# Optimization experiments

Hardware: AMD Instinct MI355X
Metric: run time of the kernel (lower is better)

The kernel has to match this reference:

```python
import jax, jax.numpy as jnp
import numpy as np
from jax import lax

B, L, D_MODEL = 2, 1024, 1024
EXPAND, D_STATE, D_CONV = 2, 16, 4
D_INNER = EXPAND * D_MODEL
DT_RANK = D_MODEL // 16  # ceil(1024/16) = 64
D_FF = 4 * D_MODEL


def setup_inputs() -> dict:
    key = jax.random.key(0)
    ks = jax.random.split(key, 20)
    s = lambda *sh: 1.0 / np.sqrt(sh[-1])
    inp = {
        "x": jax.random.normal(ks[0], (B, L, D_MODEL), jnp.float32),
        "ln1_w": jnp.ones((D_MODEL,), jnp.float32),
        "ln1_b": jnp.zeros((D_MODEL,), jnp.float32),
        "W_in": jax.random.normal(ks[1], (2 * D_INNER, D_MODEL), jnp.float32) * s(D_MODEL),
        "conv_w": jax.random.normal(ks[2], (D_INNER, D_CONV), jnp.float32) * s(D_CONV),
        "conv_b": jnp.zeros((D_INNER,), jnp.float32),
        "W_xproj": jax.random.normal(ks[3], (DT_RANK + 2 * D_STATE, D_INNER), jnp.float32) * s(D_INNER),
        "W_dt": jax.random.normal(ks[4], (D_INNER, DT_RANK), jnp.float32) * s(DT_RANK),
        "b_dt": jax.random.uniform(ks[5], (D_INNER,), jnp.float32, -4.0, -2.0),  # dt bias ~ small softplus
        "A_log": jnp.log(jnp.broadcast_to(jnp.arange(1, D_STATE + 1, dtype=jnp.float32), (D_INNER, D_STATE))),
        "D": jnp.ones((D_INNER,), jnp.float32),
        "W_out": jax.random.normal(ks[6], (D_MODEL, D_INNER), jnp.float32) * s(D_INNER),
        "ln2_w": jnp.ones((D_MODEL,), jnp.float32),
        "ln2_b": jnp.zeros((D_MODEL,), jnp.float32),
        "W1": jax.random.normal(ks[7], (D_FF, D_MODEL), jnp.float32) * s(D_MODEL),
        "b1": jnp.zeros((D_FF,), jnp.float32),
        "W2": jax.random.normal(ks[8], (D_MODEL, D_FF), jnp.float32) * s(D_FF),
        "b2": jnp.zeros((D_MODEL,), jnp.float32),
    }
    return inp


def _layernorm(x, w, b, eps=1e-5):
    mu = jnp.mean(x, axis=-1, keepdims=True)
    var = jnp.var(x, axis=-1, keepdims=True)
    return (x - mu) * lax.rsqrt(var + eps) * w + b


def _mamba(h, W_in, conv_w, conv_b, W_xproj, W_dt, b_dt, A_log, D, W_out):
    # in_proj -> [B, L, 2*d_inner]
    xz = jnp.einsum("bld,ed->ble", h, W_in)
    u, z = xz[..., :D_INNER], xz[..., D_INNER:]
    # causal depthwise conv over time
    uc = jnp.transpose(u, (0, 2, 1))  # [B, d_inner, L]
    uc = lax.conv_general_dilated(
        uc, conv_w[:, None, :], window_strides=(1,), padding=[(D_CONV - 1, 0)],
        dimension_numbers=("NCH", "OIH", "NCH"), feature_group_count=D_INNER)
    uc = jax.nn.silu(uc + conv_b[None, :, None])
    u = jnp.transpose(uc, (0, 2, 1))  # [B, L, d_inner]
    # input-dependent dt, B, C
    x_db = jnp.einsum("bld,ed->ble", u, W_xproj)
    dt = jax.nn.softplus(jnp.einsum("blr,dr->bld", x_db[..., :DT_RANK], W_dt) + b_dt)
    Bm = x_db[..., DT_RANK:DT_RANK + D_STATE]  # [B, L, d_state]
    Cm = x_db[..., DT_RANK + D_STATE:]         # [B, L, d_state]
    A = -jnp.exp(A_log)                        # [d_inner, d_state]

    def step(hst, t):
        dt_t, B_t, C_t, u_t = t  # [B,d_inner], [B,ds], [B,ds], [B,d_inner]
        dA = jnp.exp(dt_t[:, :, None] * A)                       # [B,d_inner,d_state]
        hst = dA * hst + dt_t[:, :, None] * B_t[:, None, :] * u_t[:, :, None]
        y_t = jnp.einsum("bds,bs->bd", hst, C_t)
        return hst, y_t

    h0 = jnp.zeros((u.shape[0], D_INNER, D_STATE), u.dtype)
    xs = (jnp.swapaxes(dt, 0, 1), jnp.swapaxes(Bm, 0, 1), jnp.swapaxes(Cm, 0, 1), jnp.swapaxes(u, 0, 1))
    _, ys = lax.scan(step, h0, xs)
    y = jnp.swapaxes(ys, 0, 1) + u * D  # skip term D*u
    y = y * jax.nn.silu(z)
    return jnp.einsum("ble,de->bld", y, W_out)


def reference(x, ln1_w, ln1_b, W_in, conv_w, conv_b, W_xproj, W_dt, b_dt, A_log, D,
              W_out, ln2_w, ln2_b, W1, b1, W2, b2):
    x = x + _mamba(_layernorm(x, ln1_w, ln1_b), W_in, conv_w, conv_b, W_xproj, W_dt, b_dt, A_log, D, W_out)
    h = _layernorm(x, ln2_w, ln2_b)
    ffn = jnp.einsum("blf,df->bld", jax.nn.relu(jnp.einsum("bld,fd->blf", h, W1) + b1), W2) + b2
    return x + ffn
```

## Files before the change

### kernel.cpp

```cpp
#include <hip/hip_runtime.h>

typedef unsigned short u16;
typedef unsigned int   u32;
typedef short   bf16x8 __attribute__((ext_vector_type(8)));
typedef float   f32x4  __attribute__((ext_vector_type(4)));
typedef u16     u16x4  __attribute__((ext_vector_type(4)));

__device__ __forceinline__ u16 f2b(float f) {
    u32 u = __builtin_bit_cast(u32, f);
    u32 r = u + 0x7FFFu + ((u >> 16) & 1u);
    return (u16)(r >> 16);
}
__device__ __forceinline__ float b2f(u16 h) {
    u32 u = ((u32)h) << 16;
    return __builtin_bit_cast(float, u);
}
__device__ __forceinline__ u16x4 f4_to_b4(float4 v) {
    u16x4 o; o.x = f2b(v.x); o.y = f2b(v.y); o.z = f2b(v.z); o.w = f2b(v.w);
    return o;
}

__device__ __forceinline__ float fexp2(float x) {
    float r;
    asm("v_exp_f32 %0, %1" : "=v"(r) : "v"(x));
    return r;
}
__device__ __forceinline__ float flog2(float x) {
    float r;
    asm("v_log_f32 %0, %1" : "=v"(r) : "v"(x));
    return r;
}

template <int CTRL>
__device__ __forceinline__ float dpp_add(float p) {
    int pi = __builtin_bit_cast(int, p);
    int q  = __builtin_amdgcn_update_dpp(pi, pi, CTRL, 0xF, 0xF, false);
    return p + __builtin_bit_cast(float, q);
}
#define DPP_XOR1 0xB1
#define DPP_XOR2 0x4E
#define DPP_HMIR 0x141
#define DPP_MIR  0x140

#define MROWS   2048
#define NSEG    16
#define SEGT    64
#define L2E     1.44269504088896340736f
#define LN2     0.69314718055994530942f

#define GLDS(g, l) __builtin_amdgcn_global_load_lds(                      \
    (const __attribute__((address_space(1))) void*)(g),                   \
    (__attribute__((address_space(3))) void*)(l), 16, 0, 0)

__global__ __launch_bounds__(256) void cvt_kernel(const float* __restrict__ in,
                                                  u16* __restrict__ out, int n4) {
    int i = blockIdx.x * 256 + threadIdx.x;
    if (i < n4) {
        float4 v = ((const float4*)in)[i];
        ((u16x4*)out)[i] = f4_to_b4(v);
    }
}

__global__ __launch_bounds__(256) void pad_xproj_kernel(const float* __restrict__ in,
                                                        u16* __restrict__ out) {
    int i = blockIdx.x * 256 + threadIdx.x;
    int r = i >> 9, c4 = i & 511;
    float4 v = make_float4(0.f, 0.f, 0.f, 0.f);
    if (r < 96) v = ((const float4*)(in + (size_t)r * 2048))[c4];
    ((u16x4*)(out + (size_t)r * 2048))[c4] = f4_to_b4(v);
}

__global__ __launch_bounds__(256) void ln_kernel(const float* __restrict__ x,
                                                 const float* __restrict__ w,
                                                 const float* __restrict__ b,
                                                 u16* __restrict__ out) {
    const int row = blockIdx.x;
    const int tid = threadIdx.x;
    const float4 v = ((const float4*)(x + (size_t)row * 1024))[tid];
    float s = v.x + v.y + v.z + v.w;
    float q = v.x * v.x + v.y * v.y + v.z * v.z + v.w * v.w;
#pragma unroll
    for (int off = 1; off < 64; off <<= 1) {
        s += __shfl_xor(s, off, 64);
        q += __shfl_xor(q, off, 64);
    }
    __shared__ float ss[4], qq[4];
    const int wave = tid >> 6;
    if ((tid & 63) == 0) { ss[wave] = s; qq[wave] = q; }
    __syncthreads();
    s = ss[0] + ss[1] + ss[2] + ss[3];
    q = qq[0] + qq[1] + qq[2] + qq[3];
    const float mean = s * (1.f / 1024.f);
    const float var  = q * (1.f / 1024.f) - mean * mean;
    const float rstd = rsqrtf(var + 1e-5f);
    const float4 wv = ((const float4*)w)[tid];
    const float4 bv = ((const float4*)b)[tid];
    float4 o;
    o.x = (v.x - mean) * rstd * wv.x + bv.x;
    o.y = (v.y - mean) * rstd * wv.y + bv.y;
    o.z = (v.z - mean) * rstd * wv.z + bv.z;
    o.w = (v.w - mean) * rstd * wv.w + bv.w;
    ((u16x4*)(out + (size_t)row * 1024))[tid] = f4_to_b4(o);
}

__global__ __launch_bounds__(256) void conv_kernel(const float* __restrict__ xzu,
                                                   const float* __restrict__ cw,
                                                   const float* __restrict__ cb,
                                                   u16* __restrict__ up,
                                                   u16* __restrict__ utl) {
    const int idx = blockIdx.x * 256 + threadIdx.x;
    const int row = idx >> 9;
    const int d4  = idx & 511;
    const int d   = d4 * 4;
    const int bb  = row >> 10;
    const int t   = row & 1023;
    float w0[4], w1[4], w2[4], w3[4];
    *(float4*)w0 = ((const float4*)cw)[d + 0];
    *(float4*)w1 = ((const float4*)cw)[d + 1];
    *(float4*)w2 = ((const float4*)cw)[d + 2];
    *(float4*)w3 = ((const float4*)cw)[d + 3];
    float4 a = ((const float4*)cb)[d4];
#pragma unroll
    for (int j = 0; j < 4; ++j) {
        const int tt = t - 3 + j;
        if (tt >= 0) {
            const float4 uv = *(const float4*)(xzu + ((size_t)(bb * 1024 + tt)) * 2048 + d);
            a.x += uv.x * w0[j];
            a.y += uv.y * w1[j];
            a.z += uv.z * w2[j];
            a.w += uv.w * w3[j];
        }
    }
    float4 o;
    o.x = a.x / (1.f + __expf(-a.x));
    o.y = a.y / (1.f + __expf(-a.y));
    o.z = a.z / (1.f + __expf(-a.z));
    o.w = a.w / (1.f + __expf(-a.w));
    const u16x4 pk = f4_to_b4(o);
    ((u16x4*)up)[idx] = pk;
    *(u16x4*)(utl + (((size_t)(d >> 4)) * 2048 + row) * 16 + (d & 15)) = pk;
}

template <int EPI>
__global__ __launch_bounds__(256) void gemm_tb(const u16* __restrict__ A,
                                               const u16* __restrict__ Bw,
                                               void* __restrict__ Cptr,
                                               void* __restrict__ Cptr2,
                                               const float* __restrict__ bias,
                                               int M, int N, int K, int KS) {
    const int nbm = gridDim.x, nbn = gridDim.y;
    const int nwg = nbm * nbn;
    const int id  = blockIdx.x + nbm * blockIdx.y;
    const int sw  = (id & 7) * (nwg >> 3) + (id >> 3);
    const int bm  = sw % nbm, bn = sw / nbm;

    __shared__ u16 Asm[3][128 * 32];
    __shared__ u16 Bsm[3][128 * 32];
    const int tid  = threadIdx.x;
    const int kz   = blockIdx.z;
    const int lane = tid & 63;
    const int wave = tid >> 6;
    const int wm   = wave >> 1, wn = wave & 1;
    const u16* Ag = A  + (size_t)bm * 128 * K;
    const u16* Bg = Bw + (size_t)bn * 128 * K;
    const int r0 = tid >> 2;
    const int r1 = r0 + 64;
    const int sg = (tid & 3) * 8;
    const int k0 = kz * KS;
    const int nk = KS >> 5;
    const int fr = lane & 15, fk = (lane >> 4) * 8;

#define STG(bf, kk)                                                            \
    {                                                                          \
        const int kof = k0 + (kk) * 32;                                        \
        GLDS(Ag + (size_t)r0 * K + kof + sg, &Asm[bf][tid * 8]);               \
        GLDS(Ag + (size_t)r1 * K + kof + sg, &Asm[bf][(tid + 256) * 8]);       \
        GLDS(Bg + (size_t)r0 * K + kof + sg, &Bsm[bf][tid * 8]);               \
        GLDS(Bg + (size_t)r1 * K + kof + sg, &Bsm[bf][(tid + 256) * 8]);       \
    }

    f32x4 acc[4][4] = {};
    STG(0, 0); STG(1, 1); STG(2, 2);
    int buf = 0;
    for (int k = 0; k < nk; ++k) {
        if (k < nk - 2)       asm volatile("s_waitcnt vmcnt(8)" ::: "memory");
        else if (k == nk - 2) asm volatile("s_waitcnt vmcnt(4)" ::: "memory");
        else                  asm volatile("s_waitcnt vmcnt(0)" ::: "memory");
        __builtin_amdgcn_s_barrier();
        bf16x8 a[4], b[4];
#pragma unroll
        for (int m = 0; m < 4; ++m)
            a[m] = *(const bf16x8*)&Asm[buf][(wm * 64 + m * 16 + fr) * 32 + fk];
#pragma unroll
        for (int n = 0; n < 4; ++n)
            b[n] = *(const bf16x8*)&Bsm[buf][(wn * 64 + n * 16 + fr) * 32 + fk];
        asm volatile("s_waitcnt lgkmcnt(0)" ::: "memory");
        __builtin_amdgcn_s_barrier();
        if (k + 3 < nk) STG(buf, k + 3);
#pragma unroll
        for (int m = 0; m < 4; ++m)
#pragma unroll
            for (int n = 0; n < 4; ++n)
                acc[m][n] = __builtin_amdgcn_mfma_f32_16x16x32_bf16(a[m], b[n], acc[m][n], 0, 0, 0);
        buf = (buf == 2) ? 0 : buf + 1;
    }
#undef STG

    const int fq = lane >> 4;
#pragma unroll
    for (int m = 0; m < 4; ++m) {
#pragma unroll
        for (int n = 0; n < 4; ++n) {
            const int row0 = bm * 128 + wm * 64 + m * 16 + fq * 4;
            const int col  = bn * 128 + wn * 64 + n * 16 + fr;
#pragma unroll
            for (int j = 0; j < 4; ++j) {
                float v = acc[m][n][j];
                if constexpr (EPI == 3) {
                    v += bias[col];
                    ((u16*)Cptr)[(size_t)(row0 + j) * N + col] = f2b(fmaxf(v, 0.f));
                } else if constexpr (EPI == 5) {
                    if (col < 2048) {
                        ((float*)Cptr)[(size_t)(row0 + j) * 2048 + col] = v;
                    } else {
                        const float sv = v / (1.f + __expf(-v));
                        const int zc = col - 2048;
                        ((u16*)Cptr2)[(((size_t)(zc >> 4)) * 2048 + row0 + j) * 16 + (zc & 15)]
                            = f2b(sv);
                    }
                } else {
                    ((float*)Cptr)[(size_t)kz * M * N + (size_t)(row0 + j) * N + col] = v;
                }
            }
        }
    }
}

__global__ __launch_bounds__(256) void xproj_combine(const float* __restrict__ part,
                                                     u16* __restrict__ xdbr,
                                                     float* __restrict__ bcp) {
    int i = blockIdx.x * 256 + threadIdx.x;
    int row = i >> 5, c4 = i & 31;
    if (c4 >= 24) return;
    float4 s = make_float4(0.f, 0.f, 0.f, 0.f);
#pragma unroll
    for (int p = 0; p < 8; ++p) {
        float4 v = ((const float4*)(part + (size_t)p * MROWS * 128 + (size_t)row * 128))[c4];
        s.x += v.x; s.y += v.y; s.z += v.z; s.w += v.w;
    }
    if (c4 < 16) {
        ((u16x4*)(xdbr + (size_t)row * 64))[c4] = f4_to_b4(s);
    } else {
        const int e0 = (c4 - 16) * 4;
        float sv[4] = {s.x, s.y, s.z, s.w};
#pragma unroll
        for (int j = 0; j < 4; ++j) {
            const int e = e0 + j;
            const int st  = (e < 16) ? e : (e - 16);
            const int isc = (e < 16) ? 0 : 1;
            bcp[(size_t)(row >> 1) * 64 + st * 4 + (row & 1) * 2 + isc] = sv[j];
        }
    }
}

__device__ __forceinline__ void compute_dtu_tile(const u16* __restrict__ xdbr,
                                                 const u16* __restrict__ Wdtb,
                                                 const float* __restrict__ b_dt,
                                                 const u16* __restrict__ utile,
                                                 float* __restrict__ du_s,
                                                 size_t t0, int d0, int w, int l) {
    const int fr = l & 15, fk = (l >> 4) * 8;
    const bf16x8 a0 = *(const bf16x8*)(xdbr + (t0 + w * 16 + fr) * 64 + fk);
    const bf16x8 a1 = *(const bf16x8*)(xdbr + (t0 + w * 16 + fr) * 64 + 32 + fk);
    const bf16x8 b0 = *(const bf16x8*)(Wdtb + (size_t)(d0 + fr) * 64 + fk);
    const bf16x8 b1 = *(const bf16x8*)(Wdtb + (size_t)(d0 + fr) * 64 + 32 + fk);
    const float bdt = b_dt[d0 + fr];
    f32x4 acc = {};
    acc = __builtin_amdgcn_mfma_f32_16x16x32_bf16(a0, b0, acc, 0, 0, 0);
    acc = __builtin_amdgcn_mfma_f32_16x16x32_bf16(a1, b1, acc, 0, 0, 0);
#pragma unroll
    for (int j = 0; j < 4; ++j) {
        const int row = w * 16 + (l >> 4) * 4 + j;
        float v = acc[j] + bdt;
        const float sp = flog2(1.f + fexp2(v * L2E)) * LN2;
        v = (v > 20.f) ? v : sp;
        const float uval = b2f(utile[(t0 + row) * 16 + fr]);
        float2 dv; dv.x = v; dv.y = v * uval;
        *(float2*)&du_s[(row >> 1) * 66 + fr * 4 + (row & 1) * 2] = dv;
    }
}

__device__ __forceinline__ void stage_bc(const float* __restrict__ bcp,
                                         float* __restrict__ bc_s,
                                         size_t p0, int w, int l) {
    const int pr = (w << 3) + (l >> 4);
    const int pc = (l & 15) << 2;
    GLDS(bcp + (p0 + pr) * 64 + pc,     &bc_s[(w << 9)]);
    GLDS(bcp + (p0 + pr + 4) * 64 + pc, &bc_s[(w << 9) + 256]);
}

__global__ __launch_bounds__(256) void scan_pass1(const u16* __restrict__ xdbr,
                                                  const u16* __restrict__ Wdtb,
                                                  const float* __restrict__ b_dt,
                                                  const u16* __restrict__ utl,
                                                  const float* __restrict__ bcp,
                                                  const float* __restrict__ A_log,
                                                  float* __restrict__ Qarr,
                                                  float* __restrict__ Sarr) {
    __shared__ __align__(16) float du_s[32 * 66];
    __shared__ __align__(16) float bc_s[32 * 64];

    const int tid = threadIdx.x;
    const int l   = tid & 63;
    const int w   = tid >> 6;
    const int s   = l & 15;
    const int g   = (w << 2) | (l >> 4);
    const int d0  = blockIdx.x << 4;
    const int b   = blockIdx.y;
    const int seg = blockIdx.z;
    const int d   = d0 + g;
    const size_t t0 = (size_t)b * 1024 + (size_t)seg * SEGT;
    const u16* utile = utl + (size_t)(d0 >> 4) * 2048 * 16;

    stage_bc(bcp, bc_s, t0 >> 1, w, l);
    compute_dtu_tile(xdbr, Wdtb, b_dt, utile, du_s, t0, d0, w, l);

    const float As2 = -__expf(A_log[d * 16 + s]) * L2E;
    asm volatile("s_waitcnt vmcnt(0) lgkmcnt(0)" ::: "memory");
    __builtin_amdgcn_s_barrier();

    float Q = 0.f, S = 0.f;
#pragma unroll 8
    for (int t2 = 0; t2 < 32; ++t2) {
        const float4 du4 = *(const float4*)&du_s[t2 * 66 + g * 4];
        const float4 BC2 = *(const float4*)&bc_s[t2 * 64 + s * 4];
        S += du4.x;
        Q = fexp2(du4.x * As2) * Q + du4.y * BC2.x;
        S += du4.z;
        Q = fexp2(du4.z * As2) * Q + du4.w * BC2.z;
    }
    Qarr[(((size_t)seg * 2 + b) * 2048 + d) * 16 + s] = Q;
    if (s == 0) Sarr[((size_t)seg * 2 + b) * 2048 + d] = S;
}

__global__ __launch_bounds__(256) void scan_prefix(const float* __restrict__ Qarr,
                                                   const float* __restrict__ Sarr,
                                                   const float* __restrict__ A_log,
                                                   float* __restrict__ H0) {
    const int tid = threadIdx.x;
    const int d   = (blockIdx.x << 4) + (tid >> 4);
    const int s   = tid & 15;
    const int b   = blockIdx.y;
    const float As2 = -__expf(A_log[d * 16 + s]) * L2E;
    float h = 0.f;
#pragma unroll
    for (int i = 0; i < NSEG; ++i) {
        const size_t base = ((size_t)i * 2 + b) * 2048 + d;
        H0[base * 16 + s] = h;
        h = fexp2(As2 * Sarr[base]) * h + Qarr[base * 16 + s];
    }
}

__global__ __launch_bounds__(256) void scan_pass2(const u16* __restrict__ xdbr,
                                                  const u16* __restrict__ Wdtb,
                                                  const float* __restrict__ b_dt,
                                                  const u16* __restrict__ utl,
                                                  const float* __restrict__ bcp,
                                                  const u16* __restrict__ zst,
                                                  const float* __restrict__ A_log,
                                                  const float* __restrict__ Dp,
                                                  const float* __restrict__ H0,
                                                  u16* __restrict__ ymul) {
    __shared__ __align__(16) float du_s[32 * 66];
    __shared__ __align__(16) float bc_s[32 * 64];
    __shared__ __align__(16) u16   u_s[1024];
    __shared__ __align__(16) u16   z_s[1024];

    const int tid = threadIdx.x;
    const int l   = tid & 63;
    const int w   = tid >> 6;
    const int s   = l & 15;
    const int g   = (w << 2) | (l >> 4);
    const int d0  = blockIdx.x << 4;
    const int b   = blockIdx.y;
    const int seg = blockIdx.z;
    const int d   = d0 + g;
    const size_t t0 = (size_t)b * 1024 + (size_t)seg * SEGT;
    const u16* utile = utl + (size_t)(d0 >> 4) * 2048 * 16;
    const u16* ztile = zst + (size_t)(d0 >> 4) * 2048 * 16;

    stage_bc(bcp, bc_s, t0 >> 1, w, l);
    if (w < 2)
        GLDS(utile + t0 * 16 + ((w & 1) * 64 + l) * 8, &u_s[(w & 1) << 9]);
    else
        GLDS(ztile + t0 * 16 + ((w & 1) * 64 + l) * 8, &z_s[(w & 1) << 9]);

    compute_dtu_tile(xdbr, Wdtb, b_dt, utile, du_s, t0, d0, w, l);

    const float As2 = -__expf(A_log[d * 16 + s]) * L2E;
    float h = H0[(((size_t)seg * 2 + b) * 2048 + d) * 16 + s];

    asm volatile("s_waitcnt vmcnt(0) lgkmcnt(0)" ::: "memory");
    __builtin_amdgcn_s_barrier();

    float pk[4];
#pragma unroll
    for (int c = 0; c < 4; ++c) {
        pk[c] = 0.f;
#pragma unroll
        for (int q = 0; q < 8; ++q) {
            const int t2 = c * 8 + q;
            const float4 du4 = *(const float4*)&du_s[t2 * 66 + g * 4];
            const float4 BC2 = *(const float4*)&bc_s[t2 * 64 + s * 4];
            h = fexp2(du4.x * As2) * h + du4.y * BC2.x;
            float p = h * BC2.y;
            p = dpp_add<DPP_XOR1>(p);
            p = dpp_add<DPP_XOR2>(p);
            p = dpp_add<DPP_HMIR>(p);
            p = dpp_add<DPP_MIR>(p);
            {
                const unsigned long long km = 0x0001000100010001ULL << (2 * q);
                asm("v_cndmask_b32 %0, %0, %1, %2" : "+v"(pk[c]) : "v"(p), "s"(km));
            }
            h = fexp2(du4.z * As2) * h + du4.w * BC2.z;
            p = h * BC2.w;
            p = dpp_add<DPP_XOR1>(p);
            p = dpp_add<DPP_XOR2>(p);
            p = dpp_add<DPP_HMIR>(p);
            p = dpp_add<DPP_MIR>(p);
            {
                const unsigned long long km = 0x0001000100010001ULL << (2 * q + 1);
                asm("v_cndmask_b32 %0, %0, %1, %2" : "+v"(pk[c]) : "v"(p), "s"(km));
            }
        }
    }

    __builtin_amdgcn_s_barrier();
    float* p_s = du_s;
#pragma unroll
    for (int c = 0; c < 4; ++c) {
        const int row = c * 16 + s;
        p_s[row * 16 + (g ^ (row & 12))] = pk[c];
    }

    asm volatile("s_waitcnt lgkmcnt(0)" ::: "memory");
    __builtin_amdgcn_s_barrier();

    {
        const int tt = tid >> 2, cc = (tid & 3) << 2;
        const float4 pv = *(const float4*)&p_s[tt * 16 + (cc ^ (tt & 12))];
        const u16x4  uv = *(const u16x4*)&u_s[tt * 16 + cc];
        const u16x4  zs = *(const u16x4*)&z_s[tt * 16 + cc];
        const float4 Dv = *(const float4*)(Dp + d0 + cc);
        float4 o;
        o.x = (pv.x + b2f(uv.x) * Dv.x) * b2f(zs.x);
        o.y = (pv.y + b2f(uv.y) * Dv.y) * b2f(zs.y);
        o.z = (pv.z + b2f(uv.z) * Dv.z) * b2f(zs.z);
        o.w = (pv.w + b2f(uv.w) * Dv.w) * b2f(zs.w);
        *(u16x4*)(ymul + (t0 + tt) * 2048 + d0 + cc) = f4_to_b4(o);
    }
}

__global__ __launch_bounds__(256) void ffn2_combine(const float* __restrict__ part,
                                                    const float* __restrict__ x2,
                                                    const float* __restrict__ b2,
                                                    float* __restrict__ out) {
    int i = blockIdx.x * 256 + threadIdx.x;
    float4 s = ((const float4*)x2)[i];
    float4 bv = ((const float4*)b2)[i & 255];
    s.x += bv.x; s.y += bv.y; s.z += bv.z; s.w += bv.w;
#pragma unroll
    for (int p = 0; p < 4; ++p) {
        float4 v = ((const float4*)(part + (size_t)p * MROWS * 1024))[i];
        s.x += v.x; s.y += v.y; s.z += v.z; s.w += v.w;
    }
    ((float4*)out)[i] = s;
}

__global__ __launch_bounds__(256) void outproj_combine_ln2(const float* __restrict__ x,
                                                           const float* __restrict__ part,
                                                           const float* __restrict__ w,
                                                           const float* __restrict__ b,
                                                           float* __restrict__ x2,
                                                           u16* __restrict__ h2) {
    const int row = blockIdx.x;
    const int tid = threadIdx.x;
    float4 v = ((const float4*)(x + (size_t)row * 1024))[tid];
    float4 p0 = ((const float4*)(part + (size_t)row * 1024))[tid];
    float4 p1 = ((const float4*)(part + (size_t)MROWS * 1024 + (size_t)row * 1024))[tid];
    v.x += p0.x + p1.x; v.y += p0.y + p1.y; v.z += p0.z + p1.z; v.w += p0.w + p1.w;
    ((float4*)(x2 + (size_t)row * 1024))[tid] = v;
    float s = v.x + v.y + v.z + v.w;
    float q = v.x * v.x + v.y * v.y + v.z * v.z + v.w * v.w;
#pragma unroll
    for (int off = 1; off < 64; off <<= 1) {
        s += __shfl_xor(s, off, 64);
        q += __shfl_xor(q, off, 64);
    }
    __shared__ float ss[4], qq[4];
    const int wave = tid >> 6;
    if ((tid & 63) == 0) { ss[wave] = s; qq[wave] = q; }
    __syncthreads();
    s = ss[0] + ss[1] + ss[2] + ss[3];
    q = qq[0] + qq[1] + qq[2] + qq[3];
    const float mean = s * (1.f / 1024.f);
    const float var  = q * (1.f / 1024.f) - mean * mean;
    const float rstd = rsqrtf(var + 1e-5f);
    const float4 wv = ((const float4*)w)[tid];
    const float4 bv = ((const float4*)b)[tid];
    float4 o;
    o.x = (v.x - mean) * rstd * wv.x + bv.x;
    o.y = (v.y - mean) * rstd * wv.y + bv.y;
    o.z = (v.z - mean) * rstd * wv.z + bv.z;
    o.w = (v.w - mean) * rstd * wv.w + bv.w;
    ((u16x4*)(h2 + (size_t)row * 1024))[tid] = f4_to_b4(o);
}

extern "C" void kernel_launch(void* const* d_in, const int* in_sizes, int n_in,
                              void* d_out, int out_size, void* d_ws, size_t ws_size,
                              hipStream_t stream) {
    const float* x      = (const float*)d_in[0];
    const float* ln1_w  = (const float*)d_in[1];
    const float* ln1_b  = (const float*)d_in[2];
    const float* W_in   = (const float*)d_in[3];
    const float* conv_w = (const float*)d_in[4];
    const float* conv_b = (const float*)d_in[5];
    const float* W_xproj= (const float*)d_in[6];
    const float* W_dt   = (const float*)d_in[7];
    const float* b_dt   = (const float*)d_in[8];
    const float* A_log  = (const float*)d_in[9];
    const float* Dvec   = (const float*)d_in[10];
    const float* W_out  = (const float*)d_in[11];
    const float* ln2_w  = (const float*)d_in[12];
    const float* ln2_b  = (const float*)d_in[13];
    const float* W1     = (const float*)d_in[14];
    const float* b1     = (const float*)d_in[15];
    const float* W2     = (const float*)d_in[16];
    const float* b2     = (const float*)d_in[17];
    float* out = (float*)d_out;
    char*  ws  = (char*)d_ws;
    const size_t MB = 1024ull * 1024ull;

    u16*   h1b   = (u16*)(ws + 0);
    float* xzu   = (float*)(ws + 4 * MB);
    u16*   zst   = (u16*)(ws + 20 * MB);
    u16*   upb   = (u16*)(ws + 28 * MB);
    u16*   utl   = (u16*)(ws + 36 * MB);
    float* parts = (float*)(ws + 44 * MB);
    float* bcp   = (float*)(ws + 52 * MB);
    u16*   xdbr  = (u16*)(ws + 52 * MB + 256 * 1024);
    u16*   Wdtb  = (u16*)(ws + 52 * MB + 512 * 1024);
    u16*   ymul  = (u16*)(ws + 53 * MB);
    float* Qarr  = (float*)(ws + 61 * MB);
    float* Sarr  = (float*)(ws + 65 * MB);
    float* H0    = (float*)(ws + 66 * MB);
    float* x2    = (float*)(ws + 70 * MB);
    u16*   Winb  = (u16*)(ws + 78 * MB);
    u16*   Woutb = (u16*)(ws + 86 * MB);
    u16*   W1b   = (u16*)(ws + 90 * MB);
    u16*   W2b   = (u16*)(ws + 98 * MB);
    u16*   Wxpb  = (u16*)(ws + 106 * MB);
    u16*   h2b   = h1b;
    float* opart = (float*)(ws + 4 * MB);
    u16*   f1    = (u16*)(ws + 4 * MB);
    float* fpart = (float*)(ws + 20 * MB);

    cvt_kernel<<<4096, 256, 0, stream>>>(W_in,  Winb,  4096 * 1024 / 4);
    cvt_kernel<<<2048, 256, 0, stream>>>(W_out, Woutb, 1024 * 2048 / 4);
    cvt_kernel<<<4096, 256, 0, stream>>>(W1,    W1b,   4096 * 1024 / 4);
    cvt_kernel<<<4096, 256, 0, stream>>>(W2,    W2b,   1024 * 4096 / 4);
    cvt_kernel<<<128,  256, 0, stream>>>(W_dt,  Wdtb,  2048 * 64 / 4);
    pad_xproj_kernel<<<256, 256, 0, stream>>>(W_xproj, Wxpb);

    ln_kernel<<<2048, 256, 0, stream>>>(x, ln1_w, ln1_b, h1b);
    gemm_tb<5><<<dim3(16, 32, 1), 256, 0, stream>>>(h1b, Winb, xzu, zst, nullptr,
                                                    MROWS, 4096, 1024, 1024);
    conv_kernel<<<4096, 256, 0, stream>>>(xzu, conv_w, conv_b, upb, utl);
    gemm_tb<10><<<dim3(16, 1, 8), 256, 0, stream>>>(upb, Wxpb, parts, nullptr, nullptr,
                                                    MROWS, 128, 2048, 256);
    xproj_combine<<<256, 256, 0, stream>>>(parts, xdbr, bcp);
    scan_pass1<<<dim3(128, 2, NSEG), 256, 0, stream>>>(xdbr, Wdtb, b_dt, utl, bcp, A_log,
                                                       Qarr, Sarr);
    scan_prefix<<<dim3(128, 2), 256, 0, stream>>>(Qarr, Sarr, A_log, H0);
    scan_pass2<<<dim3(128, 2, NSEG), 256, 0, stream>>>(xdbr, Wdtb, b_dt, utl, bcp, zst,
                                                       A_log, Dvec, H0, ymul);
    gemm_tb<10><<<dim3(16, 8, 2), 256, 0, stream>>>(ymul, Woutb, opart, nullptr, nullptr,
                                                    MROWS, 1024, 2048, 1024);
    outproj_combine_ln2<<<2048, 256, 0, stream>>>(x, opart, ln2_w, ln2_b, x2, h2b);
    gemm_tb<3><<<dim3(16, 32, 1), 256, 0, stream>>>(h2b, W1b, f1, nullptr, b1,
                                                    MROWS, 4096, 1024, 1024);
    gemm_tb<10><<<dim3(16, 8, 4), 256, 0, stream>>>(f1, W2b, fpart, nullptr, nullptr,
                                                    MROWS, 1024, 4096, 1024);
    ffn2_combine<<<2048, 256, 0, stream>>>(fpart, x2, b2, out);
}
```

Measured before the change: 234.7 us.

## Replace split-K GEMMs with 64x64-tile GEMM fusing residual and bias epilogue

Adds a 64x64-tile bf16 MFMA GEMM with a three-stage LDS pipeline that writes output plus residual (and bias) directly. It replaces the split-K out_proj and FFN2 GEMMs and their combine kernels, so the fp32 partial buffers are never written and re-read and two launches are dropped. LN2 now runs through the generic ln_kernel on x2. The cost is more tiles, each with a full-length K loop (2048 or 4096), and less data reuse per tile than the 128-wide version.

```diff
diff --git a/kernel.cpp b/kernel.cpp
--- a/kernel.cpp
+++ b/kernel.cpp
@@ -230,6 +230,95 @@
                     }
                 } else {
                     ((float*)Cptr)[(size_t)kz * M * N + (size_t)(row0 + j) * N + col] = v;
+                }
+            }
+        }
+    }
+}
+
+template <int EPI>
+__global__ __launch_bounds__(256) void gemm64(const u16* __restrict__ A,
+                                              const u16* __restrict__ Bw,
+                                              float* __restrict__ Cptr,
+                                              const float* __restrict__ bias,
+                                              const float* __restrict__ resid,
+                                              int M, int N, int K) {
+    const int nbm = gridDim.x, nbn = gridDim.y;
+    const int nwg = nbm * nbn;
+    const int id  = blockIdx.x + nbm * blockIdx.y;
+    const int sw  = (id & 7) * (nwg >> 3) + (id >> 3);
+    const int bm  = sw % nbm, bn = sw / nbm;
+
+    __shared__ u16 Asm[3][2][64 * 32];
+    __shared__ u16 Bsm[3][2][64 * 32];
+    const int tid  = threadIdx.x;
+    const int lane = tid & 63;
+    const int wave = tid >> 6;
+    const int wm   = wave >> 1, wn = wave & 1;
+    const u16* Ag = A  + (size_t)bm * 64 * K;
+    const u16* Bg = Bw + (size_t)bn * 64 * K;
+    const int r0 = tid >> 2;
+    const int sg = (tid & 3) * 8;
+    const int nk = K >> 6;
+    const int fr = lane & 15, fk = (lane >> 4) * 8;
+
+#define STG64(bf, kk)                                                          \
+    {                                                                          \
+        const int kof = (kk) * 64;                                             \
+        GLDS(Ag + (size_t)r0 * K + kof + sg,      &Asm[bf][0][tid * 8]);       \
+        GLDS(Ag + (size_t)r0 * K + kof + 32 + sg, &Asm[bf][1][tid * 8]);       \
+        GLDS(Bg + (size_t)r0 * K + kof + sg,      &Bsm[bf][0][tid * 8]);       \
+        GLDS(Bg + (size_t)r0 * K + kof + 32 + sg, &Bsm[bf][1][tid * 8]);       \
+    }
+
+    f32x4 acc[2][2] = {};
+    STG64(0, 0); STG64(1, 1); STG64(2, 2);
+    int buf = 0;
+    for (int k = 0; k < nk; ++k) {
+        if (k < nk - 2)       asm volatile("s_waitcnt vmcnt(8)" ::: "memory");
+        else if (k == nk - 2) asm volatile("s_waitcnt vmcnt(4)" ::: "memory");
+        else                  asm volatile("s_waitcnt vmcnt(0)" ::: "memory");
+        __builtin_amdgcn_s_barrier();
+        bf16x8 a[2][2], b[2][2];
+#pragma unroll
+        for (int kk = 0; kk < 2; ++kk) {
+#pragma unroll
+            for (int m = 0; m < 2; ++m)
+                a[kk][m] = *(const bf16x8*)&Asm[buf][kk][(wm * 32 + m * 16 + fr) * 32 + fk];
+#pragma unroll
+            for (int n = 0; n < 2; ++n)
+                b[kk][n] = *(const bf16x8*)&Bsm[buf][kk][(wn * 32 + n * 16 + fr) * 32 + fk];
+        }
+        asm volatile("s_waitcnt lgkmcnt(0)" ::: "memory");
+        __builtin_amdgcn_s_barrier();
+        if (k + 3 < nk) STG64(buf, k + 3);
+#pragma unroll
+        for (int kk = 0; kk < 2; ++kk)
+#pragma unroll
+            for (int m = 0; m < 2; ++m)
+#pragma unroll
+                for (int n = 0; n < 2; ++n)
+                    acc[m][n] = __builtin_amdgcn_mfma_f32_16x16x32_bf16(a[kk][m], b[kk][n],
+                                                                        acc[m][n], 0, 0, 0);
+        buf = (buf == 2) ? 0 : buf + 1;
+    }
+#undef STG64
+
+    const int fq = lane >> 4;
+#pragma unroll
+    for (int m = 0; m < 2; ++m) {
+#pragma unroll
+        for (int n = 0; n < 2; ++n) {
+            const int row0 = bm * 64 + wm * 32 + m * 16 + fq * 4;
+            const int col  = bn * 64 + wn * 32 + n * 16 + fr;
+#pragma unroll
+            for (int j = 0; j < 4; ++j) {
+                float v = acc[m][n][j];
+                const size_t off = (size_t)(row0 + j) * N + col;
+                if constexpr (EPI == 6) {
+                    Cptr[off] = v + bias[col] + resid[off];
+                } else {
+                    Cptr[off] = v + resid[off];
                 }
             }
         }
@@ -461,61 +550,6 @@
     }
 }
 
-__global__ __launch_bounds__(256) void ffn2_combine(const float* __restrict__ part,
-                                                    const float* __restrict__ x2,
-                                                    const float* __restrict__ b2,
-                                                    float* __restrict__ out) {
-    int i = blockIdx.x * 256 + threadIdx.x;
-    float4 s = ((const float4*)x2)[i];
-    float4 bv = ((const float4*)b2)[i & 255];
-    s.x += bv.x; s.y += bv.y; s.z += bv.z; s.w += bv.w;
-#pragma unroll
-    for (int p = 0; p < 4; ++p) {
-        float4 v = ((const float4*)(part + (size_t)p * MROWS * 1024))[i];
-        s.x += v.x; s.y += v.y; s.z += v.z; s.w += v.w;
-    }
-    ((float4*)out)[i] = s;
-}
-
-__global__ __launch_bounds__(256) void outproj_combine_ln2(const float* __restrict__ x,
-                                                           const float* __restrict__ part,
-                                                           const float* __restrict__ w,
-                                                           const float* __restrict__ b,
-                                                           float* __restrict__ x2,
-                                                           u16* __restrict__ h2) {
-    const int row = blockIdx.x;
-    const int tid = threadIdx.x;
-    float4 v = ((const float4*)(x + (size_t)row * 1024))[tid];
-    float4 p0 = ((const float4*)(part + (size_t)row * 1024))[tid];
-    float4 p1 = ((const float4*)(part + (size_t)MROWS * 1024 + (size_t)row * 1024))[tid];
-    v.x += p0.x + p1.x; v.y += p0.y + p1.y; v.z += p0.z + p1.z; v.w += p0.w + p1.w;
-    ((float4*)(x2 + (size_t)row * 1024))[tid] = v;
-    float s = v.x + v.y + v.z + v.w;
-    float q = v.x * v.x + v.y * v.y + v.z * v.z + v.w * v.w;
-#pragma unroll
-    for (int off = 1; off < 64; off <<= 1) {
-        s += __shfl_xor(s, off, 64);
-        q += __shfl_xor(q, off, 64);
-    }
-    __shared__ float ss[4], qq[4];
-    const int wave = tid >> 6;
-    if ((tid & 63) == 0) { ss[wave] = s; qq[wave] = q; }
-    __syncthreads();
-    s = ss[0] + ss[1] + ss[2] + ss[3];
-    q = qq[0] + qq[1] + qq[2] + qq[3];
-    const float mean = s * (1.f / 1024.f);
-    const float var  = q * (1.f / 1024.f) - mean * mean;
-    const float rstd = rsqrtf(var + 1e-5f);
-    const float4 wv = ((const float4*)w)[tid];
-    const float4 bv = ((const float4*)b)[tid];
-    float4 o;
-    o.x = (v.x - mean) * rstd * wv.x + bv.x;
-    o.y = (v.y - mean) * rstd * wv.y + bv.y;
-    o.z = (v.z - mean) * rstd * wv.z + bv.z;
-    o.w = (v.w - mean) * rstd * wv.w + bv.w;
-    ((u16x4*)(h2 + (size_t)row * 1024))[tid] = f4_to_b4(o);
-}
-
 extern "C" void kernel_launch(void* const* d_in, const int* in_sizes, int n_in,
                               void* d_out, int out_size, void* d_ws, size_t ws_size,
                               hipStream_t stream) {
@@ -561,9 +595,7 @@
     u16*   W2b   = (u16*)(ws + 98 * MB);
     u16*   Wxpb  = (u16*)(ws + 106 * MB);
     u16*   h2b   = h1b;
-    float* opart = (float*)(ws + 4 * MB);
     u16*   f1    = (u16*)(ws + 4 * MB);
-    float* fpart = (float*)(ws + 20 * MB);
 
     cvt_kernel<<<4096, 256, 0, stream>>>(W_in,  Winb,  4096 * 1024 / 4);
     cvt_kernel<<<2048, 256, 0, stream>>>(W_out, Woutb, 1024 * 2048 / 4);
@@ -584,12 +616,11 @@
     scan_prefix<<<dim3(128, 2), 256, 0, stream>>>(Qarr, Sarr, A_log, H0);
     scan_pass2<<<dim3(128, 2, NSEG), 256, 0, stream>>>(xdbr, Wdtb, b_dt, utl, bcp, zst,
                                                        A_log, Dvec, H0, ymul);
-    gemm_tb<10><<<dim3(16, 8, 2), 256, 0, stream>>>(ymul, Woutb, opart, nullptr, nullptr,
-                                                    MROWS, 1024, 2048, 1024);
-    outproj_combine_ln2<<<2048, 256, 0, stream>>>(x, opart, ln2_w, ln2_b, x2, h2b);
+    gemm64<7><<<dim3(32, 16), 256, 0, stream>>>(ymul, Woutb, x2, nullptr, x,
+                                                MROWS, 1024, 2048);
+    ln_kernel<<<2048, 256, 0, stream>>>(x2, ln2_w, ln2_b, h2b);
     gemm_tb<3><<<dim3(16, 32, 1), 256, 0, stream>>>(h2b, W1b, f1, nullptr, b1,
                                                     MROWS, 4096, 1024, 1024);
-    gemm_tb<10><<<dim3(16, 8, 4), 256, 0, stream>>>(f1, W2b, fpart, nullptr, nullptr,
-                                                    MROWS, 1024, 4096, 1024);
-    ffn2_combine<<<2048, 256, 0, stream>>>(fpart, x2, b2, out);
-}
+    gemm64<6><<<dim3(32, 16), 256, 0, stream>>>(f1, W2b, out, b2, x2,
+                                                MROWS, 1024, 4096);
+}
```

Result: no change. 238.7 us (+1.7%).

## Use 64x128 tiles for the wide GEMMs and store the in_proj u-half as bf16

Applied to the files above, without the earlier changes.

Adds a gemm_a64 kernel with a 64-row by 128-column tile, launched as a 32x32 grid, for the in_proj and FFN1 GEMMs (N=4096). This gives 1024 workgroups instead of 512, which should fill the CUs better. The u half of the in_proj output is now written as bf16 instead of fp32, and the conv kernel reads bf16, halving that intermediate's memory traffic. The split-K gemm_tb is reduced to plain fp32 partial output. The cost is lower data reuse per tile and an extra bf16 rounding of u before the convolution.

```diff
diff --git a/kernel.cpp b/kernel.cpp
--- a/kernel.cpp
+++ b/kernel.cpp
@@ -103,7 +103,7 @@
     ((u16x4*)(out + (size_t)row * 1024))[tid] = f4_to_b4(o);
 }
 
-__global__ __launch_bounds__(256) void conv_kernel(const float* __restrict__ xzu,
+__global__ __launch_bounds__(256) void conv_kernel(const u16* __restrict__ xzu,
                                                    const float* __restrict__ cw,
                                                    const float* __restrict__ cb,
                                                    u16* __restrict__ up,
@@ -124,11 +124,11 @@
     for (int j = 0; j < 4; ++j) {
         const int tt = t - 3 + j;
         if (tt >= 0) {
-            const float4 uv = *(const float4*)(xzu + ((size_t)(bb * 1024 + tt)) * 2048 + d);
-            a.x += uv.x * w0[j];
-            a.y += uv.y * w1[j];
-            a.z += uv.z * w2[j];
-            a.w += uv.w * w3[j];
+            const u16x4 uv = *(const u16x4*)(xzu + ((size_t)(bb * 1024 + tt)) * 2048 + d);
+            a.x += b2f(uv.x) * w0[j];
+            a.y += b2f(uv.y) * w1[j];
+            a.z += b2f(uv.z) * w2[j];
+            a.w += b2f(uv.w) * w3[j];
         }
     }
     float4 o;
@@ -141,17 +141,14 @@
     *(u16x4*)(utl + (((size_t)(d >> 4)) * 2048 + row) * 16 + (d & 15)) = pk;
 }
 
-template <int EPI>
 __global__ __launch_bounds__(256) void gemm_tb(const u16* __restrict__ A,
                                                const u16* __restrict__ Bw,
-                                               void* __restrict__ Cptr,
-                                               void* __restrict__ Cptr2,
-                                               const float* __restrict__ bias,
+                                               float* __restrict__ Cptr,
                                                int M, int N, int K, int KS) {
     const int nbm = gridDim.x, nbn = gridDim.y;
     const int nwg = nbm * nbn;
     const int id  = blockIdx.x + nbm * blockIdx.y;
-    const int sw  = (id & 7) * (nwg >> 3) + (id >> 3);
+    const int sw  = (nwg >= 8) ? ((id & 7) * (nwg >> 3) + (id >> 3)) : id;
     const int bm  = sw % nbm, bn = sw / nbm;
 
     __shared__ u16 Asm[3][128 * 32];
@@ -214,22 +211,96 @@
             const int row0 = bm * 128 + wm * 64 + m * 16 + fq * 4;
             const int col  = bn * 128 + wn * 64 + n * 16 + fr;
 #pragma unroll
+            for (int j = 0; j < 4; ++j)
+                Cptr[(size_t)kz * M * N + (size_t)(row0 + j) * N + col] = acc[m][n][j];
+        }
+    }
+}
+
+template <int EPI>
+__global__ __launch_bounds__(256) void gemm_a64(const u16* __restrict__ A,
+                                                const u16* __restrict__ Bw,
+                                                void* __restrict__ Cptr,
+                                                void* __restrict__ Cptr2,
+                                                const float* __restrict__ bias,
+                                                int M, int N, int K) {
+    const int nbm = gridDim.x, nbn = gridDim.y;
+    const int nwg = nbm * nbn;
+    const int id  = blockIdx.x + nbm * blockIdx.y;
+    const int sw  = (id & 7) * (nwg >> 3) + (id >> 3);
+    const int bm  = sw % nbm, bn = sw / nbm;
+
+    __shared__ u16 Asm[3][64 * 32];
+    __shared__ u16 Bsm[3][128 * 32];
+    const int tid  = threadIdx.x;
+    const int lane = tid & 63;
+    const int wave = tid >> 6;
+    const int wm   = wave >> 1, wn = wave & 1;
+    const u16* Ag = A  + (size_t)bm * 64 * K;
+    const u16* Bg = Bw + (size_t)bn * 128 * K;
+    const int r0 = tid >> 2;
+    const int r1 = r0 + 64;
+    const int sg = (tid & 3) * 8;
+    const int nk = K >> 5;
+    const int fr = lane & 15, fk = (lane >> 4) * 8;
+
+#define STGA(bf, kk)                                                           \
+    {                                                                          \
+        const int kof = (kk) * 32;                                             \
+        GLDS(Ag + (size_t)r0 * K + kof + sg, &Asm[bf][tid * 8]);               \
+        GLDS(Bg + (size_t)r0 * K + kof + sg, &Bsm[bf][tid * 8]);               \
+        GLDS(Bg + (size_t)r1 * K + kof + sg, &Bsm[bf][(tid + 256) * 8]);       \
+    }
+
+    f32x4 acc[2][4] = {};
+    STGA(0, 0); STGA(1, 1); STGA(2, 2);
+    int buf = 0;
+    for (int k = 0; k < nk; ++k) {
+        if (k < nk - 2)       asm volatile("s_waitcnt vmcnt(6)" ::: "memory");
+        else if (k == nk - 2) asm volatile("s_waitcnt vmcnt(3)" ::: "memory");
+        else                  asm volatile("s_waitcnt vmcnt(0)" ::: "memory");
+        __builtin_amdgcn_s_barrier();
+        bf16x8 a[2], b[4];
+#pragma unroll
+        for (int m = 0; m < 2; ++m)
+            a[m] = *(const bf16x8*)&Asm[buf][(wm * 32 + m * 16 + fr) * 32 + fk];
+#pragma unroll
+        for (int n = 0; n < 4; ++n)
+            b[n] = *(const bf16x8*)&Bsm[buf][(wn * 64 + n * 16 + fr) * 32 + fk];
+        asm volatile("s_waitcnt lgkmcnt(0)" ::: "memory");
+        __builtin_amdgcn_s_barrier();
+        if (k + 3 < nk) STGA(buf, k + 3);
+#pragma unroll
+        for (int m = 0; m < 2; ++m)
+#pragma unroll
+            for (int n = 0; n < 4; ++n)
+                acc[m][n] = __builtin_amdgcn_mfma_f32_16x16x32_bf16(a[m], b[n], acc[m][n], 0, 0, 0);
+        buf = (buf == 2) ? 0 : buf + 1;
+    }
+#undef STGA
+
+    const int fq = lane >> 4;
+#pragma unroll
+    for (int m = 0; m < 2; ++m) {
+#pragma unroll
+        for (int n = 0; n < 4; ++n) {
+            const int row0 = bm * 64 + wm * 32 + m * 16 + fq * 4;
+            const int col  = bn * 128 + wn * 64 + n * 16 + fr;
+#pragma unroll
             for (int j = 0; j < 4; ++j) {
                 float v = acc[m][n][j];
                 if constexpr (EPI == 3) {
                     v += bias[col];
                     ((u16*)Cptr)[(size_t)(row0 + j) * N + col] = f2b(fmaxf(v, 0.f));
-                } else if constexpr (EPI == 5) {
+                } else {
                     if (col < 2048) {
-                        ((float*)Cptr)[(size_t)(row0 + j) * 2048 + col] = v;
+                        ((u16*)Cptr)[(size_t)(row0 + j) * 2048 + col] = f2b(v);
                     } else {
                         const float sv = v / (1.f + __expf(-v));
                         const int zc = col - 2048;
                         ((u16*)Cptr2)[(((size_t)(zc >> 4)) * 2048 + row0 + j) * 16 + (zc & 15)]
                             = f2b(sv);
                     }
-                } else {
-                    ((float*)Cptr)[(size_t)kz * M * N + (size_t)(row0 + j) * N + col] = v;
                 }
             }
         }
@@ -542,24 +613,24 @@
     const size_t MB = 1024ull * 1024ull;
 
     u16*   h1b   = (u16*)(ws + 0);
-    float* xzu   = (float*)(ws + 4 * MB);
-    u16*   zst   = (u16*)(ws + 20 * MB);
-    u16*   upb   = (u16*)(ws + 28 * MB);
-    u16*   utl   = (u16*)(ws + 36 * MB);
-    float* parts = (float*)(ws + 44 * MB);
-    float* bcp   = (float*)(ws + 52 * MB);
-    u16*   xdbr  = (u16*)(ws + 52 * MB + 256 * 1024);
-    u16*   Wdtb  = (u16*)(ws + 52 * MB + 512 * 1024);
-    u16*   ymul  = (u16*)(ws + 53 * MB);
-    float* Qarr  = (float*)(ws + 61 * MB);
-    float* Sarr  = (float*)(ws + 65 * MB);
-    float* H0    = (float*)(ws + 66 * MB);
-    float* x2    = (float*)(ws + 70 * MB);
-    u16*   Winb  = (u16*)(ws + 78 * MB);
-    u16*   Woutb = (u16*)(ws + 86 * MB);
-    u16*   W1b   = (u16*)(ws + 90 * MB);
-    u16*   W2b   = (u16*)(ws + 98 * MB);
-    u16*   Wxpb  = (u16*)(ws + 106 * MB);
+    u16*   xzu   = (u16*)(ws + 4 * MB);
+    u16*   zst   = (u16*)(ws + 12 * MB);
+    u16*   upb   = (u16*)(ws + 20 * MB);
+    u16*   utl   = (u16*)(ws + 28 * MB);
+    float* parts = (float*)(ws + 36 * MB);
+    float* bcp   = (float*)(ws + 44 * MB);
+    u16*   xdbr  = (u16*)(ws + 44 * MB + 256 * 1024);
+    u16*   Wdtb  = (u16*)(ws + 44 * MB + 512 * 1024);
+    u16*   ymul  = (u16*)(ws + 45 * MB);
+    float* Qarr  = (float*)(ws + 53 * MB);
+    float* Sarr  = (float*)(ws + 57 * MB);
+    float* H0    = (float*)(ws + 58 * MB);
+    float* x2    = (float*)(ws + 62 * MB);
+    u16*   Winb  = (u16*)(ws + 70 * MB);
+    u16*   Woutb = (u16*)(ws + 78 * MB);
+    u16*   W1b   = (u16*)(ws + 82 * MB);
+    u16*   W2b   = (u16*)(ws + 90 * MB);
+    u16*   Wxpb  = (u16*)(ws + 98 * MB);
     u16*   h2b   = h1b;
     float* opart = (float*)(ws + 4 * MB);
     u16*   f1    = (u16*)(ws + 4 * MB);
@@ -573,23 +644,20 @@
     pad_xproj_kernel<<<256, 256, 0, stream>>>(W_xproj, Wxpb);
 
     ln_kernel<<<2048, 256, 0, stream>>>(x, ln1_w, ln1_b, h1b);
-    gemm_tb<5><<<dim3(16, 32, 1), 256, 0, stream>>>(h1b, Winb, xzu, zst, nullptr,
-                                                    MROWS, 4096, 1024, 1024);
+    gemm_a64<5><<<dim3(32, 32), 256, 0, stream>>>(h1b, Winb, xzu, zst, nullptr,
+                                                  MROWS, 4096, 1024);
     conv_kernel<<<4096, 256, 0, stream>>>(xzu, conv_w, conv_b, upb, utl);
-    gemm_tb<10><<<dim3(16, 1, 8), 256, 0, stream>>>(upb, Wxpb, parts, nullptr, nullptr,
-                                                    MROWS, 128, 2048, 256);
+    gemm_tb<<<dim3(16, 1, 8), 256, 0, stream>>>(upb, Wxpb, parts, MROWS, 128, 2048, 256);
     xproj_combine<<<256, 256, 0, stream>>>(parts, xdbr, bcp);
     scan_pass1<<<dim3(128, 2, NSEG), 256, 0, stream>>>(xdbr, Wdtb, b_dt, utl, bcp, A_log,
                                                        Qarr, Sarr);
     scan_prefix<<<dim3(128, 2), 256, 0, stream>>>(Qarr, Sarr, A_log, H0);
     scan_pass2<<<dim3(128, 2, NSEG), 256, 0, stream>>>(xdbr, Wdtb, b_dt, utl, bcp, zst,
                                                        A_log, Dvec, H0, ymul);
-    gemm_tb<10><<<dim3(16, 8, 2), 256, 0, stream>>>(ymul, Woutb, opart, nullptr, nullptr,
-                                                    MROWS, 1024, 2048, 1024);
+    gemm_tb<<<dim3(16, 8, 2), 256, 0, stream>>>(ymul, Woutb, opart, MROWS, 1024, 2048, 1024);
     outproj_combine_ln2<<<2048, 256, 0, stream>>>(x, opart, ln2_w, ln2_b, x2, h2b);
-    gemm_tb<3><<<dim3(16, 32, 1), 256, 0, stream>>>(h2b, W1b, f1, nullptr, b1,
-                                                    MROWS, 4096, 1024, 1024);
-    gemm_tb<10><<<dim3(16, 8, 4), 256, 0, stream>>>(f1, W2b, fpart, nullptr, nullptr,
-                                                    MROWS, 1024, 4096, 1024);
+    gemm_a64<3><<<dim3(32, 32), 256, 0, stream>>>(h2b, W1b, f1, nullptr, b1,
+                                                  MROWS, 4096, 1024);
+    gemm_tb<<<dim3(16, 8, 4), 256, 0, stream>>>(f1, W2b, fpart, MROWS, 1024, 4096, 1024);
     ffn2_combine<<<2048, 256, 0, stream>>>(fpart, x2, b2, out);
 }
```

Measured after the change: 242.9 us. 3.5% more time.
